# Kernel optimization log

Measured on AMD Instinct MI355X. Metric: run time of the kernel, lower is better.

Reference implementation:

```python
import jax, jax.numpy as jnp
import numpy as np

LX, LY = 256, 256
K_CLASSES = 4
N_SWEEPS = 2
N_SITES = LX * LY

# 8-neighborhood offsets (Moore neighborhood), border handled by clipping
_OFFSETS = np.array([[-1, -1], [-1, 0], [-1, 1],
                     [0, -1],           [0, 1],
                     [1, -1],  [1, 0],  [1, 1]], dtype=np.int32)


def setup_inputs() -> dict:
    key = jax.random.key(0)
    k1, k2, k3, k4 = jax.random.split(key, 4)
    X_init = jax.random.randint(k1, (LX, LY), 0, K_CLASSES).astype(jnp.int32)
    perm = jax.random.permutation(k2, jnp.arange(N_SITES)).astype(jnp.int32)
    uniforms = jax.random.uniform(k3, (N_SWEEPS, N_SITES), dtype=jnp.float32)
    beta = jax.random.uniform(k4, (), dtype=jnp.float32) + 0.5  # Potts coupling
    return {"X_init": X_init, "perm": perm, "uniforms": uniforms,
            "beta": beta, "K": K_CLASSES}


def reference(X_init, perm, uniforms, beta, K):
    lx, ly = X_init.shape
    off = jnp.asarray(_OFFSETS)              # (8, 2)
    classes = jnp.arange(K)                  # (K,)

    def update_one_site(X, uv, r):
        u, v = jnp.unravel_index(uv, (lx, ly))
        uu = jnp.clip(u + off[:, 0], 0, lx - 1)   # (8,) neighbor rows
        vv = jnp.clip(v + off[:, 1], 0, ly - 1)   # (8,) neighbor cols
        neigh = X[uu, vv]                          # (8,) dynamic gather
        # Potts potential: p_k proportional to exp(beta * #{neighbors == k})
        counts = (neigh[None, :] == classes[:, None]).sum(axis=1)  # (K,)
        probs = jax.nn.softmax(beta * counts.astype(jnp.float32))  # (K,) sums to 1
        # inverse-CDF categorical sample, as in the original cumsum < r
        x_sample = jnp.count_nonzero(jnp.cumsum(probs) < r)
        return X.at[u, v].set(x_sample.astype(X.dtype))  # scatter write

    def one_sweep(X, rs):
        def body(Xc, inp):
            uv, r = inp
            return update_one_site(Xc, uv, r), None
        X, _ = jax.lax.scan(body, X, (perm, rs))
        return X, None

    X_final, _ = jax.lax.scan(one_sweep, X_init, uniforms)  # N_SWEEPS sweeps
    return X_final
```

## Files before the change

### kernel.cpp

```cpp
#include <hip/hip_runtime.h>
#include <math.h>

#define NSITES 65536
#define WIN 8192
#define NW 8
#define KN 8
#define RMAX 64


__device__ __forceinline__ int agg_pos(int v, int* c, int vmax) {
  int pos = 0;
  const int lane = threadIdx.x & 63;
  for (int vv = 1; vv <= vmax; ++vv) {
    unsigned long long m = __ballot(v == vv);
    if (m) {
      int leader = __ffsll((long long)m) - 1;
      int base = 0;
      if (lane == leader) base = atomicAdd(&c[vv], (int)__popcll(m));
      base = __shfl(base, leader);
      if (v == vv) pos = base + (int)__popcll(m & ((1ull << lane) - 1ull));
    }
  }
  return pos;
}

__global__ __launch_bounds__(1024) void GibbsPred_kernel(
    const int* __restrict__ perm, uint4* __restrict__ preds) {
  __shared__ unsigned short posg[NSITES];
  const int tid = threadIdx.x;
  const int w = blockIdx.x >> 3;
  const int c = blockIdx.x & 7;
  const int wbase = w * WIN;

  for (int g = tid; g < NSITES / 8; g += 1024)
    ((uint4*)posg)[g] = make_uint4(0u, 0u, 0u, 0u);
  __syncthreads();

#pragma unroll
  for (int k = 0; k < KN; ++k) {
    const int lt = k * 1024 + tid;
    posg[perm[wbase + lt]] = (unsigned short)(lt + 1);
  }
  __syncthreads();

  const int lt = c * 1024 + tid;
  const int uv = perm[wbase + lt], u = uv >> 8, v = uv & 255;
  const int um = u ? u - 1 : 0, up = u < 255 ? u + 1 : 255;
  const int vm = v ? v - 1 : 0, vp = v < 255 ? v + 1 : 255;
  const int nb8[8] = {(um << 8) | vm, (um << 8) | v, (um << 8) | vp,
                      (u << 8) | vm,                 (u << 8) | vp,
                      (up << 8) | vm, (up << 8) | v, (up << 8) | vp};
  unsigned short pl[8];
  int np = 0;
#pragma unroll
  for (int j = 0; j < 8; ++j) {
    const int p = posg[nb8[j]];
    if (p && p - 1 < lt) pl[np++] = (unsigned short)(p - 1);
  }
  for (int j = np; j < 8; ++j) pl[j] = 0xFFFF;
  preds[wbase + lt] =
      make_uint4((unsigned)pl[0] | ((unsigned)pl[1] << 16),
                 (unsigned)pl[2] | ((unsigned)pl[3] << 16),
                 (unsigned)pl[4] | ((unsigned)pl[5] << 16),
                 (unsigned)pl[6] | ((unsigned)pl[7] << 16));
}

__global__ __launch_bounds__(1024) void GibbsSched_kernel(
    const int* __restrict__ perm, const float* __restrict__ uni,
    const uint4* __restrict__ preds, uint2* __restrict__ recpk,
    int* __restrict__ ends) {
  __shared__ unsigned short lvl[WIN];
  __shared__ int cnt[RMAX + 1], coff[RMAX + 1];
  __shared__ int chg, bmax;
  const int tid = threadIdx.x;
  const int w = blockIdx.x;
  const int wbase = w * WIN;

  for (int i = tid; i <= RMAX; i += 1024) { cnt[i] = 0; coff[i] = 0; }
  if (tid == 0) bmax = 0;
  __syncthreads();

  int myl[KN];
  for (int c = 0; c < KN; ++c) {
    const int lt = c * 1024 + tid;
    const uint4 pp = preds[wbase + lt];
    const unsigned ent[8] = {pp.x & 0xFFFFu, pp.x >> 16, pp.y & 0xFFFFu,
                             pp.y >> 16,     pp.z & 0xFFFFu, pp.z >> 16,
                             pp.w & 0xFFFFu, pp.w >> 16};
    int basemax = 0;
    unsigned short intr[8];
    int nin = 0;
#pragma unroll
    for (int j = 0; j < 8; ++j) {
      const unsigned p = ent[j];
      if (p == 0xFFFFu) continue;
      if ((int)p < c * 1024) basemax = max(basemax, (int)lvl[p]);
      else intr[nin++] = (unsigned short)p;
    }
    int ml = basemax + 1;
    lvl[lt] = (unsigned short)ml;
    __syncthreads();

    for (;;) {
      if (tid == 0) chg = 0;
      __syncthreads();
      bool ch = false;
      if (nin) {
        int m = basemax;
        for (int j = 0; j < nin; ++j) m = max(m, (int)lvl[intr[j]]);
        const int nl = m + 1;
        if (nl != ml) { ml = nl; lvl[lt] = (unsigned short)nl; ch = true; }
      }
      if (ch) chg = 1;
      __syncthreads();
      if (chg == 0) break;
    }
    myl[c] = ml;
  }

#pragma unroll
  for (int k = 0; k < KN; ++k) atomicMax(&bmax, myl[k]);
  __syncthreads();
  const int vmax = bmax;

#pragma unroll
  for (int k = 0; k < KN; ++k) (void)agg_pos(myl[k], cnt, vmax);
  __syncthreads();
  if (tid == 0) {
    int e = 0;
    for (int r = 0; r < RMAX; ++r) {
      coff[r] = e;
      e += cnt[r];
      ends[w * RMAX + r] = e;
    }
  }
  __syncthreads();

#pragma unroll
  for (int k = 0; k < KN; ++k) {
    const int pos = agg_pos(myl[k], coff, vmax);
    const int lt = tid + k * 1024;
    const int gp = wbase + pos;
    const unsigned uvv = (unsigned)perm[wbase + lt];
    recpk[gp] = make_uint2(uvv, __float_as_uint(uni[wbase + lt]));
    recpk[NSITES + gp] =
        make_uint2(uvv, __float_as_uint(uni[NSITES + wbase + lt]));
  }
}

__device__ __forceinline__ void do_update(unsigned char* cell,
                                          const unsigned int* cellw,
                                          const float* c0a, const float* c1a,
                                          const float* c2a, const float* c3a,
                                          unsigned uvv, float r) {
  const int u = uvv >> 8, v = (int)(uvv & 255u);
  const int um = u ? u - 1 : 0, up = u < 255 ? u + 1 : 255;
  const int vm = v ? v - 1 : 0, vp = v < 255 ? v + 1 : 255;
  const int cb = vm >> 2;
  const int sh0 = (vm & 3) << 3;
  const int shv = (v - vm) << 3;
  const int shp = (vp - vm) << 3;
  int acc = 0;
  {
    const unsigned int* rw = cellw + (um << 6) + cb;
    const unsigned long long wd =
        ((unsigned long long)rw[1] << 32) | (unsigned long long)rw[0];
    const unsigned wl = (unsigned)(wd >> sh0);
    acc += 1 << ((wl & 255u) << 2);
    acc += 1 << (((wl >> shv) & 255u) << 2);
    acc += 1 << (((wl >> shp) & 255u) << 2);
  }
  {
    const unsigned int* rw = cellw + (u << 6) + cb;
    const unsigned long long wd =
        ((unsigned long long)rw[1] << 32) | (unsigned long long)rw[0];
    const unsigned wl = (unsigned)(wd >> sh0);
    acc += 1 << ((wl & 255u) << 2);
    acc += 1 << (((wl >> shp) & 255u) << 2);
  }
  {
    const unsigned int* rw = cellw + (up << 6) + cb;
    const unsigned long long wd =
        ((unsigned long long)rw[1] << 32) | (unsigned long long)rw[0];
    const unsigned wl = (unsigned)(wd >> sh0);
    acc += 1 << ((wl & 255u) << 2);
    acc += 1 << (((wl >> shv) & 255u) << 2);
    acc += 1 << (((wl >> shp) & 255u) << 2);
  }
  const int n0 = acc & 15, n1 = (acc >> 4) & 15, n2 = (acc >> 8) & 15;
  const int idx = n0 + 9 * n1 + 81 * n2;
  int cnt = (c0a[idx] < r) ? 1 : 0;
  cnt += (c1a[idx] < r) ? 1 : 0;
  cnt += (c2a[idx] < r) ? 1 : 0;
  cnt += (c3a[idx] < r) ? 1 : 0;
  cell[uvv] = (unsigned char)cnt;
}

__global__ __launch_bounds__(1024) void GibbsSampler_90443421319469_kernel(
    const int* __restrict__ Xi, const uint2* __restrict__ recpk,
    const float* __restrict__ betap, const int* __restrict__ ends,
    int* __restrict__ out) {
#pragma clang fp contract(off)
  __shared__ __align__(16) unsigned int cellw[NSITES / 4];
  __shared__ float c0a[729], c1a[729], c2a[729], c3a[729];
  __shared__ int lend[NW * RMAX];
  unsigned char* cell = (unsigned char*)cellw;
  const int tid = threadIdx.x;
  const float beta = betap[0];

  for (int g = tid; g < NSITES / 4; g += 1024) {
    int4 x = ((const int4*)Xi)[g];
    cellw[g] = (unsigned)(x.x & 255) | ((unsigned)(x.y & 255) << 8) |
               ((unsigned)(x.z & 255) << 16) | ((unsigned)(x.w & 255) << 24);
  }
  if (tid < NW * RMAX) lend[tid] = ends[tid];
  for (int t = tid; t < 729; t += 1024) {
    const int n0 = t % 9, n1 = (t / 9) % 9, n2 = t / 81;
    const int n3 = 8 - n0 - n1 - n2;
    float v0 = 2.f, v1 = 2.f, v2 = 2.f, v3 = 2.f;
    if (n3 >= 0) {
      const int mx = max(max(n0, n1), max(n2, n3));
      const float xm = beta * (float)mx;
      const float x0 = beta * (float)n0;
      const float x1 = beta * (float)n1;
      const float x2 = beta * (float)n2;
      const float x3 = beta * (float)n3;
      const float e0 = (float)exp((double)(x0 - xm));
      const float e1 = (float)exp((double)(x1 - xm));
      const float e2 = (float)exp((double)(x2 - xm));
      const float e3 = (float)exp((double)(x3 - xm));
      const float s = ((e0 + e1) + e2) + e3;
      v0 = e0 / s;
      v1 = v0 + e1 / s;
      v2 = v1 + e2 / s;
      v3 = v2 + e3 / s;
    }
    c0a[t] = v0; c1a[t] = v1; c2a[t] = v2; c3a[t] = v3;
  }
  __syncthreads();

  for (int w = 0; w < 2 * NW; ++w) {
    const int ww = w & (NW - 1);
    const int sw = w >> 3;
    const uint2* rp = recpk + sw * NSITES + ww * WIN;
    const int* le = &lend[ww * RMAX];

    int nb = 0, ne = le[1];
    uint2 cur = make_uint2(0u, 0u);
    if (tid < ne) cur = rp[tid];

    for (int rd = 1; rd < RMAX; ++rd) {
      const int b = nb, e = ne;
      if (b >= WIN) break;

      if (WIN - b <= 64) {
        if (tid < 64) {
          const int i = b + tid;
          int myrd = 0;
          uint2 rc = make_uint2(0u, 0u);
          if (i < WIN) {
            myrd = rd;
            while (le[myrd] <= i) ++myrd;
            rc = rp[i];
          }
          int mx = myrd;
#pragma unroll
          for (int off = 1; off < 64; off <<= 1)
            mx = max(mx, __shfl_xor(mx, off));
          for (int rr = rd; rr <= mx; ++rr) {
            if (myrd == rr)
              do_update(cell, cellw, c0a, c1a, c2a, c3a, rc.x,
                        __uint_as_float(rc.y));
          }
        }
        __syncthreads();
        break;
      }

      nb = e;
      ne = (rd + 1 < RMAX) ? le[rd + 1] : e;
      uint2 nxt = make_uint2(0u, 0u);
      if (nb + tid < ne) nxt = rp[nb + tid];
      if (b + tid < e)
        do_update(cell, cellw, c0a, c1a, c2a, c3a, cur.x,
                  __uint_as_float(cur.y));
      for (int i = b + tid + 1024; i < e; i += 1024) {
        const uint2 rc = rp[i];
        do_update(cell, cellw, c0a, c1a, c2a, c3a, rc.x,
                  __uint_as_float(rc.y));
      }
      __syncthreads();
      cur = nxt;
    }
  }

  for (int g = tid; g < NSITES / 4; g += 1024) {
    const unsigned p = cellw[g];
    int4 o;
    o.x = (int)(p & 255u);
    o.y = (int)((p >> 8) & 255u);
    o.z = (int)((p >> 16) & 255u);
    o.w = (int)((p >> 24) & 255u);
    ((int4*)out)[g] = o;
  }
}

extern "C" void kernel_launch(void* const* d_in, const int* in_sizes, int n_in,
                              void* d_out, int out_size, void* d_ws,
                              size_t ws_size, hipStream_t stream) {
  const int* Xi = (const int*)d_in[0];
  const int* perm = (const int*)d_in[1];
  const float* uni = (const float*)d_in[2];
  const float* beta = (const float*)d_in[3];
  int* out = (int*)d_out;

  char* ws = (char*)d_ws;
  uint2* recpk = (uint2*)ws;
  int* ends = (int*)(ws + 2 * NSITES * 8);
  uint4* preds = (uint4*)(ws + 2 * NSITES * 8 + 4096);

  GibbsPred_kernel<<<dim3(NW * 8), dim3(1024), 0, stream>>>(perm, preds);
  GibbsSched_kernel<<<dim3(NW), dim3(1024), 0, stream>>>(perm, uni, preds,
                                                         recpk, ends);
  GibbsSampler_90443421319469_kernel<<<dim3(1), dim3(1024), 0, stream>>>(
      Xi, recpk, beta, ends, out);
}
```

Baseline: 248.5 us.

## Fuse predecessor computation into scheduling kernel and stage records in LDS

Removes the separate predecessor kernel. The scheduling kernel now builds the per-window position map in shared memory and derives each site's earlier neighbours inline, which drops one kernel launch and a global round trip through the preds buffer. Output records are scattered into shared memory reusing the posg buffer, then copied to global with coalesced 16-byte stores. This adds 128KB of shared memory per block, with only 8 blocks doing the work previously spread over 64.

```diff
diff --git a/kernel.cpp b/kernel.cpp
--- a/kernel.cpp
+++ b/kernel.cpp
@@ -24,51 +24,10 @@
   return pos;
 }
 
-__global__ __launch_bounds__(1024) void GibbsPred_kernel(
-    const int* __restrict__ perm, uint4* __restrict__ preds) {
-  __shared__ unsigned short posg[NSITES];
-  const int tid = threadIdx.x;
-  const int w = blockIdx.x >> 3;
-  const int c = blockIdx.x & 7;
-  const int wbase = w * WIN;
-
-  for (int g = tid; g < NSITES / 8; g += 1024)
-    ((uint4*)posg)[g] = make_uint4(0u, 0u, 0u, 0u);
-  __syncthreads();
-
-#pragma unroll
-  for (int k = 0; k < KN; ++k) {
-    const int lt = k * 1024 + tid;
-    posg[perm[wbase + lt]] = (unsigned short)(lt + 1);
-  }
-  __syncthreads();
-
-  const int lt = c * 1024 + tid;
-  const int uv = perm[wbase + lt], u = uv >> 8, v = uv & 255;
-  const int um = u ? u - 1 : 0, up = u < 255 ? u + 1 : 255;
-  const int vm = v ? v - 1 : 0, vp = v < 255 ? v + 1 : 255;
-  const int nb8[8] = {(um << 8) | vm, (um << 8) | v, (um << 8) | vp,
-                      (u << 8) | vm,                 (u << 8) | vp,
-                      (up << 8) | vm, (up << 8) | v, (up << 8) | vp};
-  unsigned short pl[8];
-  int np = 0;
-#pragma unroll
-  for (int j = 0; j < 8; ++j) {
-    const int p = posg[nb8[j]];
-    if (p && p - 1 < lt) pl[np++] = (unsigned short)(p - 1);
-  }
-  for (int j = np; j < 8; ++j) pl[j] = 0xFFFF;
-  preds[wbase + lt] =
-      make_uint4((unsigned)pl[0] | ((unsigned)pl[1] << 16),
-                 (unsigned)pl[2] | ((unsigned)pl[3] << 16),
-                 (unsigned)pl[4] | ((unsigned)pl[5] << 16),
-                 (unsigned)pl[6] | ((unsigned)pl[7] << 16));
-}
-
 __global__ __launch_bounds__(1024) void GibbsSched_kernel(
     const int* __restrict__ perm, const float* __restrict__ uni,
-    const uint4* __restrict__ preds, uint2* __restrict__ recpk,
-    int* __restrict__ ends) {
+    uint2* __restrict__ recpk, int* __restrict__ ends) {
+  __shared__ __align__(16) unsigned short posg[NSITES];
   __shared__ unsigned short lvl[WIN];
   __shared__ int cnt[RMAX + 1], coff[RMAX + 1];
   __shared__ int chg, bmax;
@@ -76,26 +35,40 @@
   const int w = blockIdx.x;
   const int wbase = w * WIN;
 
+  for (int g = tid; g < NSITES / 8; g += 1024)
+    ((uint4*)posg)[g] = make_uint4(0u, 0u, 0u, 0u);
   for (int i = tid; i <= RMAX; i += 1024) { cnt[i] = 0; coff[i] = 0; }
   if (tid == 0) bmax = 0;
+  __syncthreads();
+
+  int uvk[KN];
+#pragma unroll
+  for (int k = 0; k < KN; ++k) {
+    const int lt = k * 1024 + tid;
+    uvk[k] = perm[wbase + lt];
+    posg[uvk[k]] = (unsigned short)(lt + 1);
+  }
   __syncthreads();
 
   int myl[KN];
   for (int c = 0; c < KN; ++c) {
     const int lt = c * 1024 + tid;
-    const uint4 pp = preds[wbase + lt];
-    const unsigned ent[8] = {pp.x & 0xFFFFu, pp.x >> 16, pp.y & 0xFFFFu,
-                             pp.y >> 16,     pp.z & 0xFFFFu, pp.z >> 16,
-                             pp.w & 0xFFFFu, pp.w >> 16};
+    const int uv = uvk[c], u = uv >> 8, v = uv & 255;
+    const int um = u ? u - 1 : 0, up = u < 255 ? u + 1 : 255;
+    const int vm = v ? v - 1 : 0, vp = v < 255 ? v + 1 : 255;
+    const int nb8[8] = {(um << 8) | vm, (um << 8) | v, (um << 8) | vp,
+                        (u << 8) | vm,                 (u << 8) | vp,
+                        (up << 8) | vm, (up << 8) | v, (up << 8) | vp};
     int basemax = 0;
     unsigned short intr[8];
     int nin = 0;
 #pragma unroll
     for (int j = 0; j < 8; ++j) {
-      const unsigned p = ent[j];
-      if (p == 0xFFFFu) continue;
-      if ((int)p < c * 1024) basemax = max(basemax, (int)lvl[p]);
-      else intr[nin++] = (unsigned short)p;
+      const int p = posg[nb8[j]];
+      if (p && p - 1 < lt) {
+        if (p - 1 < c * 1024) basemax = max(basemax, (int)lvl[p - 1]);
+        else intr[nin++] = (unsigned short)(p - 1);
+      }
     }
     int ml = basemax + 1;
     lvl[lt] = (unsigned short)ml;
@@ -136,15 +109,23 @@
   }
   __syncthreads();
 
+  uint2* srec = (uint2*)posg;
 #pragma unroll
   for (int k = 0; k < KN; ++k) {
     const int pos = agg_pos(myl[k], coff, vmax);
-    const int lt = tid + k * 1024;
-    const int gp = wbase + pos;
-    const unsigned uvv = (unsigned)perm[wbase + lt];
-    recpk[gp] = make_uint2(uvv, __float_as_uint(uni[wbase + lt]));
-    recpk[NSITES + gp] =
-        make_uint2(uvv, __float_as_uint(uni[NSITES + wbase + lt]));
+    const int lt = k * 1024 + tid;
+    srec[pos] = make_uint2((unsigned)uvk[k], __float_as_uint(uni[wbase + lt]));
+    srec[WIN + pos] =
+        make_uint2((unsigned)uvk[k], __float_as_uint(uni[NSITES + wbase + lt]));
+  }
+  __syncthreads();
+
+  const uint4* s4 = (const uint4*)srec;
+  uint4* d0 = (uint4*)(recpk + wbase);
+  uint4* d1 = (uint4*)(recpk + NSITES + wbase);
+  for (int g = tid; g < WIN / 2; g += 1024) {
+    d0[g] = s4[g];
+    d1[g] = s4[WIN / 2 + g];
   }
 }
 
@@ -317,11 +298,9 @@
   char* ws = (char*)d_ws;
   uint2* recpk = (uint2*)ws;
   int* ends = (int*)(ws + 2 * NSITES * 8);
-  uint4* preds = (uint4*)(ws + 2 * NSITES * 8 + 4096);
-
-  GibbsPred_kernel<<<dim3(NW * 8), dim3(1024), 0, stream>>>(perm, preds);
-  GibbsSched_kernel<<<dim3(NW), dim3(1024), 0, stream>>>(perm, uni, preds,
-                                                         recpk, ends);
+
+  GibbsSched_kernel<<<dim3(NW), dim3(1024), 0, stream>>>(perm, uni, recpk,
+                                                         ends);
   GibbsSampler_90443421319469_kernel<<<dim3(1), dim3(1024), 0, stream>>>(
       Xi, recpk, beta, ends, out);
 }
```

New measurement: 250.5 us. About the same (+0.8%).
